# Kernel optimization log

Measured on AMD Instinct MI355X. Metric: run time of the kernel, lower is better.

Reference implementation:

```python
import jax, jax.numpy as jnp
import numpy as np

B, N, D, H = 4, 2048, 512, 8
HD = D // H
NUM_BUCKETS, MAX_EXACT, MAX_DIST = 44, 28, 2048
_BAND_RANGES = [range(38, 44), range(34, 40), range(28, 35), range(20, 28),
                range(13, 21), range(7, 14), range(3, 9), range(0, 6)]


def _band_mask():
    m = np.zeros((NUM_BUCKETS, H), dtype=np.float32)
    for h, band in enumerate(_BAND_RANGES):
        for j in band:
            m[j, h] = 1.0
    return jnp.asarray(m)


def _rel_bucket(n):
    # T5-style causal relative-position buckets: exact for d<MAX_EXACT, log-spaced above.
    i = jnp.arange(n)[:, None]
    j = jnp.arange(n)[None, :]
    d = jnp.maximum(i - j, 0)
    safe = jnp.maximum(d, 1).astype(jnp.float32)
    logb = MAX_EXACT + (jnp.log(safe / MAX_EXACT)
                        / np.log(MAX_DIST / MAX_EXACT)
                        * (NUM_BUCKETS - MAX_EXACT)).astype(jnp.int32)
    return jnp.where(d < MAX_EXACT, d, jnp.minimum(logb, NUM_BUCKETS - 1))  # [n,n]


def setup_inputs() -> dict:
    key = jax.random.key(0)
    ks = jax.random.split(key, 12)
    s = 0.02
    return {
        "x": jax.random.normal(ks[0], (B, N, D), jnp.float32),
        "k_delta": jax.random.normal(ks[1], (B, H, N, HD), jnp.float32) * 0.1,
        "v_delta": jax.random.normal(ks[2], (B, H, N, HD), jnp.float32) * 0.1,
        "qkv_w": jax.random.normal(ks[3], (D, 3 * D), jnp.float32) * s,
        "qkv_b": jnp.zeros((3 * D,), jnp.float32),
        "gate_w": jax.random.normal(ks[4], (D, D), jnp.float32) * s,
        "gate_b": jnp.zeros((D,), jnp.float32),
        "out_w": jax.random.normal(ks[5], (D, D), jnp.float32) * s,
        "out_b": jnp.zeros((D,), jnp.float32),
        "pos_bias": jax.random.normal(ks[6], (NUM_BUCKETS, H), jnp.float32) * 0.1,
        "if_gain": jnp.ones((H,), jnp.float32),
    }


def reference(x, k_delta, v_delta, qkv_w, qkv_b, gate_w, gate_b,
              out_w, out_b, pos_bias, if_gain):
    b, n, d = x.shape
    band = _band_mask()
    # hard per-head banding of the relative bias
    eff_bias = pos_bias * band + (1.0 - band) * (-100.0)           # [44,H]
    qkv = x @ qkv_w + qkv_b                                         # [B,N,3D]
    q, k, v = jnp.split(qkv, 3, axis=-1)
    q = q.reshape(b, n, H, HD).transpose(0, 2, 1, 3)                # [B,H,N,HD]
    k = k.reshape(b, n, H, HD).transpose(0, 2, 1, 3) + k_delta
    v = v.reshape(b, n, H, HD).transpose(0, 2, 1, 3) + v_delta
    bucket = _rel_bucket(n)                                         # [N,N] int
    bias = eff_bias[bucket].transpose(2, 0, 1)                      # [H,N,N]
    scores = jnp.einsum("bhid,bhjd->bhij", q, k) / np.sqrt(HD) + bias[None]
    causal = jnp.tril(jnp.ones((n, n), bool))
    scores = jnp.where(causal[None, None], scores, -1e9)
    attn = jax.nn.softmax(scores, axis=-1)
    out = jnp.einsum("bhij,bhjd->bhid", attn, v)                    # [B,H,N,HD]
    out = out * if_gain[None, :, None, None]                        # IF gain
    out_flat = out.transpose(0, 2, 1, 3).reshape(b, n, d)
    gate = jax.nn.sigmoid(x @ gate_w + gate_b)                      # output gating
    return (out_flat * gate) @ out_w + out_b
```

## Files before the change

kernel.cpp:

```cpp
#include <hip/hip_runtime.h>
#include <cmath>

typedef unsigned short u16;
typedef unsigned short u16x4 __attribute__((ext_vector_type(4)));
typedef unsigned short u16x8 __attribute__((ext_vector_type(8)));
typedef __bf16 bf16x8 __attribute__((ext_vector_type(8)));
typedef float f32x4 __attribute__((ext_vector_type(4)));

#define HNUM 8
#define HDIM 64
#define BATCH 4
#define NSEQ 2048
#define DMODEL 512
#define LP 72
#define CPE 264
#define NSLOT 14

__device__ __forceinline__ u16 f2bf(float f) {
  unsigned int u = __builtin_bit_cast(unsigned int, f);
  u += 0x7fffu + ((u >> 16) & 1u);
  return (u16)(u >> 16);
}

__device__ __forceinline__ float bf2f(u16 v) {
  unsigned int u = ((unsigned int)v) << 16;
  return __builtin_bit_cast(float, u);
}

__device__ __forceinline__ f32x4 mfma_bf16(u16x8 a, u16x8 b, f32x4 c) {
  return __builtin_amdgcn_mfma_f32_16x16x32_bf16(
      __builtin_bit_cast(bf16x8, a), __builtin_bit_cast(bf16x8, b), c, 0, 0, 0);
}

__device__ __forceinline__ void gload16(u16* lds, const u16* g) {
  __builtin_amdgcn_global_load_lds(
      (const __attribute__((address_space(1))) void*)g,
      (__attribute__((address_space(3))) void*)lds, 16, 0, 0);
}

__device__ __forceinline__ int swz_off(int row, int lg) {
  return row * 32 + ((lg ^ ((row >> 1) & 3)) << 3);
}

template <int ROWS>
__device__ __forceinline__ void stage_tile(u16* lds, const u16* g, int tid) {
  #pragma unroll
  for (int i = 0; i < ROWS / 64; ++i) {
    const int t = i * 256 + tid;
    const int row = t >> 2;
    const int ch = (t & 3) ^ ((row >> 1) & 3);
    gload16(lds + t * 8, g + (size_t)row * DMODEL + ch * 8);
  }
}

__device__ __forceinline__ void stageAB(u16* ldsA, u16* ldsB, const u16* gA,
                                        const u16* gB, int tid) {
  {
    const int s = tid;
    const int row = s >> 2;
    const int ch = (s & 3) ^ ((row >> 1) & 3);
    gload16(ldsA + s * 8, gA + (size_t)row * DMODEL + ch * 8);
  }
  #pragma unroll
  for (int i = 0; i < 2; ++i) {
    const int s = i * 512 + tid;
    const int row = s >> 2;
    const int ch = (s & 3) ^ ((row >> 1) & 3);
    gload16(ldsB + s * 8, gB + (size_t)row * DMODEL + ch * 8);
  }
}

__global__ __launch_bounds__(256) void cvt_bf16_kernel(
    const float* __restrict__ in, u16* __restrict__ out, int n8) {
  int i = blockIdx.x * 256 + threadIdx.x;
  if (i >= n8) return;
  const float4 f0 = *(const float4*)(in + i * 8);
  const float4 f1 = *(const float4*)(in + i * 8 + 4);
  u16x8 pk;
  pk[0] = f2bf(f0.x); pk[1] = f2bf(f0.y); pk[2] = f2bf(f0.z); pk[3] = f2bf(f0.w);
  pk[4] = f2bf(f1.x); pk[5] = f2bf(f1.y); pk[6] = f2bf(f1.z); pk[7] = f2bf(f1.w);
  *(u16x8*)(out + i * 8) = pk;
}

__global__ __launch_bounds__(256) void transpose_wall(
    const float* __restrict__ qkv_w, const float* __restrict__ gate_w,
    const float* __restrict__ out_w, u16* __restrict__ fused_wt,
    u16* __restrict__ out_wt) {
  __shared__ float tile[32][33];
  const int bx = blockIdx.x;
  const float* W;
  u16* Wt;
  int N, nb;
  if (bx < 48)      { W = qkv_w;  Wt = fused_wt;                     N = 1536; nb = bx; }
  else if (bx < 64) { W = gate_w; Wt = fused_wt + (size_t)1536 * 512; N = 512;  nb = bx - 48; }
  else              { W = out_w;  Wt = out_wt;                       N = 512;  nb = bx - 64; }
  const int n0 = nb * 32, k0 = blockIdx.y * 32;
  const int tx = threadIdx.x & 31, ty = threadIdx.x >> 5;
  #pragma unroll
  for (int yy = ty; yy < 32; yy += 8)
    tile[yy][tx] = W[(size_t)(k0 + yy) * N + n0 + tx];
  __syncthreads();
  #pragma unroll
  for (int yy = ty; yy < 32; yy += 8)
    Wt[(size_t)(n0 + yy) * DMODEL + k0 + tx] = f2bf(tile[tx][yy]);
}

__global__ __launch_bounds__(256) void transpose_v_kernel(
    const u16* __restrict__ v, u16* __restrict__ vT) {
  __shared__ u16 t[64][LP];
  const int n0 = blockIdx.x * 64;
  const size_t bh = blockIdx.y;
  const int r = threadIdx.x >> 2, c0 = (threadIdx.x & 3) << 4;
  const u16* src = v + (bh * NSEQ + n0 + r) * HDIM + c0;
  u16x8 a0 = *(const u16x8*)src;
  u16x8 a1 = *(const u16x8*)(src + 8);
  #pragma unroll
  for (int j = 0; j < 8; ++j) {
    t[c0 + j][r] = a0[j];
    t[c0 + 8 + j][r] = a1[j];
  }
  __syncthreads();
  u16x8 o0 = *(const u16x8*)&t[r][c0];
  u16x8 o1 = *(const u16x8*)&t[r][c0 + 8];
  u16* dst = vT + (bh * HDIM + r) * NSEQ + n0 + c0;
  *(u16x8*)dst = o0;
  *(u16x8*)(dst + 8) = o1;
}

__global__ __launch_bounds__(256) void bias_tab_kernel(
    const float* __restrict__ pos_bias, float* __restrict__ tab) {
  int d = blockIdx.x * 256 + threadIdx.x;
  if (d >= NSEQ) return;
  int bkt;
  if (d < 28) {
    bkt = d;
  } else {
    double t = log((double)d / 28.0) / log(2048.0 / 28.0) * 16.0;
    int ti = 28 + (int)t;
    bkt = ti < 43 ? ti : 43;
  }
  const int lo[8] = {38, 34, 28, 20, 13, 7, 3, 0};
  const int hi[8] = {44, 40, 35, 28, 21, 14, 9, 6};
  #pragma unroll
  for (int h = 0; h < HNUM; ++h) {
    bool inb = (bkt >= lo[h]) && (bkt < hi[h]);
    tab[h * NSEQ + d] = inb ? pos_bias[bkt * HNUM + h] : -100.0f;
  }
}

__global__ __launch_bounds__(512, 4) void gemm_fused(
    const u16* __restrict__ Abf, const u16* __restrict__ Wt,
    const float* __restrict__ qkv_b, const float* __restrict__ gate_b,
    const float* __restrict__ kdelta, const float* __restrict__ vdelta,
    u16* __restrict__ qbf, u16* __restrict__ kbf, u16* __restrict__ vbf,
    u16* __restrict__ gate) {
  __shared__ __align__(16) u16 S[36864];
  u16* SA3[3] = {S, S + 4096, S + 8192};
  u16* SB3[3] = {S + 12288, S + 20480, S + 28672};

  const int bid = blockIdx.x;
  const int xcd = bid & 7, loc = bid >> 3;
  const int m0 = (xcd * 8 + (loc & 7)) * 128;
  const int n0 = (loc >> 3) * 256;

  const int tid = threadIdx.x;
  const int w = tid >> 6, l = tid & 63, li = l & 15, lg = l >> 4;
  const int wm = w >> 2, wn = w & 3;

  f32x4 acc[4][4];
  #pragma unroll
  for (int i = 0; i < 4; ++i)
    #pragma unroll
    for (int j = 0; j < 4; ++j) acc[i][j] = f32x4{0.f, 0.f, 0.f, 0.f};

  const u16* Ab = Abf + (size_t)m0 * DMODEL;
  const u16* Bb = Wt + (size_t)n0 * DMODEL;

  stageAB(SA3[0], SB3[0], Ab, Bb, tid);
  stageAB(SA3[1], SB3[1], Ab + 32, Bb + 32, tid);

  #pragma unroll
  for (int kt = 0; kt < 16; ++kt) {
    if (kt <= 14) asm volatile("s_waitcnt vmcnt(3)" ::: "memory");
    else          asm volatile("s_waitcnt vmcnt(0)" ::: "memory");
    __builtin_amdgcn_s_barrier();
    __builtin_amdgcn_sched_barrier(0);
    if (kt + 2 < 16)
      stageAB(SA3[(kt + 2) % 3], SB3[(kt + 2) % 3],
              Ab + (kt + 2) * 32, Bb + (kt + 2) * 32, tid);
    const u16* Asb = SA3[kt % 3];
    const u16* Bsb = SB3[kt % 3];
    u16x8 af[4], bfr[4];
    #pragma unroll
    for (int mt = 0; mt < 4; ++mt)
      af[mt] = *(const u16x8*)&Asb[swz_off(wm * 64 + mt * 16 + li, lg)];
    #pragma unroll
    for (int nt = 0; nt < 4; ++nt)
      bfr[nt] = *(const u16x8*)&Bsb[swz_off(wn * 64 + nt * 16 + li, lg)];
    asm volatile("s_waitcnt lgkmcnt(0)" ::: "memory");
    __builtin_amdgcn_sched_barrier(0);
    #pragma unroll
    for (int mt = 0; mt < 4; ++mt)
      #pragma unroll
      for (int nt = 0; nt < 4; ++nt)
        acc[mt][nt] = mfma_bf16(af[mt], bfr[nt], acc[mt][nt]);
  }
  __syncthreads();

  u16* Ct = S;
  const int seg = n0 >> 9;
  const int nin = n0 & 511;
  #pragma unroll
  for (int nt = 0; nt < 4; ++nt) {
    const int col = wn * 64 + nt * 16 + li;
    const int colg = n0 + col;
    const float bv = (seg < 3) ? qkv_b[colg] : gate_b[colg & 511];
    #pragma unroll
    for (int mt = 0; mt < 4; ++mt) {
      const int row = wm * 64 + mt * 16 + lg * 4;
      #pragma unroll
      for (int r = 0; r < 4; ++r)
        Ct[(row + r) * CPE + col] = f2bf(acc[mt][nt][r] + bv);
    }
  }
  __syncthreads();

  #pragma unroll
  for (int p = 0; p < 8; ++p) {
    const int idx = p * 512 + tid;
    const int row = idx >> 5, ccol = (idx & 31) * 8;
    const int rg = m0 + row;
    const int bb = rg >> 11, n = rg & 2047;
    u16x8 cv = *(const u16x8*)&Ct[row * CPE + ccol];
    const int cws = nin + ccol;
    if (seg == 3) {
      u16x8 o;
      #pragma unroll
      for (int j = 0; j < 8; ++j)
        o[j] = f2bf(1.f / (1.f + __expf(-bf2f(cv[j]))));
      *(u16x8*)&gate[(size_t)rg * DMODEL + cws] = o;
    } else {
      const int hh = cws >> 6, hd = cws & 63;
      const size_t hidx = (((size_t)bb * HNUM + hh) * NSEQ + n) * HDIM + hd;
      if (seg == 0) {
        u16x8 o;
        #pragma unroll
        for (int j = 0; j < 8; ++j) o[j] = f2bf(bf2f(cv[j]) * 0.125f);
        *(u16x8*)&qbf[hidx] = o;
      } else {
        const float* dp = (seg == 1 ? kdelta : vdelta) + hidx;
        float4 d0 = *(const float4*)dp;
        float4 d1 = *(const float4*)(dp + 4);
        u16x8 o;
        o[0] = f2bf(bf2f(cv[0]) + d0.x); o[1] = f2bf(bf2f(cv[1]) + d0.y);
        o[2] = f2bf(bf2f(cv[2]) + d0.z); o[3] = f2bf(bf2f(cv[3]) + d0.w);
        o[4] = f2bf(bf2f(cv[4]) + d1.x); o[5] = f2bf(bf2f(cv[5]) + d1.y);
        o[6] = f2bf(bf2f(cv[6]) + d1.z); o[7] = f2bf(bf2f(cv[7]) + d1.w);
        *(u16x8*)&((seg == 1) ? kbf : vbf)[hidx] = o;
      }
    }
  }
}

__global__ __launch_bounds__(256) void gemm_out(
    const u16* __restrict__ Abf, const u16* __restrict__ Wt,
    const float* __restrict__ bias, float* __restrict__ outf) {
  __shared__ __align__(16) u16 As[3][64 * 32];
  __shared__ __align__(16) u16 Bs[3][128 * 32];

  const int m0 = blockIdx.y * 64, n0 = blockIdx.x * 128;
  const int tid = threadIdx.x;
  const int w = tid >> 6, l = tid & 63, li = l & 15, lg = l >> 4;
  const int wr = w >> 1, wc = w & 1;

  f32x4 acc[2][4];
  #pragma unroll
  for (int i = 0; i < 2; ++i)
    #pragma unroll
    for (int j = 0; j < 4; ++j) acc[i][j] = f32x4{0.f, 0.f, 0.f, 0.f};

  const u16* Ab = Abf + (size_t)m0 * DMODEL;
  const u16* Bb = Wt + (size_t)n0 * DMODEL;

  stage_tile<64>(As[0], Ab, tid);
  stage_tile<128>(Bs[0], Bb, tid);
  stage_tile<64>(As[1], Ab + 32, tid);
  stage_tile<128>(Bs[1], Bb + 32, tid);

  #pragma unroll
  for (int kt = 0; kt < 16; ++kt) {
    if (kt <= 14) asm volatile("s_waitcnt vmcnt(3)" ::: "memory");
    else          asm volatile("s_waitcnt vmcnt(0)" ::: "memory");
    __builtin_amdgcn_s_barrier();
    __builtin_amdgcn_sched_barrier(0);
    if (kt + 2 < 16) {
      stage_tile<64>(As[(kt + 2) % 3], Ab + (kt + 2) * 32, tid);
      stage_tile<128>(Bs[(kt + 2) % 3], Bb + (kt + 2) * 32, tid);
    }
    const u16* Asb = As[kt % 3];
    const u16* Bsb = Bs[kt % 3];
    u16x8 af[2], bfr[4];
    #pragma unroll
    for (int mt = 0; mt < 2; ++mt)
      af[mt] = *(const u16x8*)&Asb[swz_off(wr * 32 + mt * 16 + li, lg)];
    #pragma unroll
    for (int nt = 0; nt < 4; ++nt)
      bfr[nt] = *(const u16x8*)&Bsb[swz_off(wc * 64 + nt * 16 + li, lg)];
    asm volatile("s_waitcnt lgkmcnt(0)" ::: "memory");
    __builtin_amdgcn_sched_barrier(0);
    #pragma unroll
    for (int mt = 0; mt < 2; ++mt)
      #pragma unroll
      for (int nt = 0; nt < 4; ++nt)
        acc[mt][nt] = mfma_bf16(af[mt], bfr[nt], acc[mt][nt]);
  }

  #pragma unroll
  for (int nt = 0; nt < 4; ++nt) {
    const int colg = n0 + wc * 64 + nt * 16 + li;
    const float bv = bias[colg];
    #pragma unroll
    for (int mt = 0; mt < 2; ++mt) {
      #pragma unroll
      for (int r = 0; r < 4; ++r) {
        const int rowg = m0 + wr * 32 + mt * 16 + lg * 4 + r;
        outf[(size_t)rowg * DMODEL + colg] = acc[mt][nt][r] + bv;
      }
    }
  }
}

__global__ __launch_bounds__(256) void attn_kernel(
    const u16* __restrict__ qbf, const u16* __restrict__ kbf,
    const u16* __restrict__ vbfT, const float* __restrict__ bias_tab,
    const float* __restrict__ if_gain, const u16* __restrict__ gate,
    u16* __restrict__ attn_out, u16* __restrict__ partO,
    float* __restrict__ partM, float* __restrict__ partL) {
  __shared__ __align__(16) u16 Ks[64][LP];
  __shared__ __align__(16) u16 Vt[64][LP];
  __shared__ __align__(16) u16 Pl[4][16][LP];

  static const int DMINW[8] = {408, 139, 26, 18, 11, 5, 1, 0};
  static const int DMAXW[8] = {2049, 702, 185, 29, 22, 15, 10, 7};
  static const int DMINS[8] = {412, 143, 30, 22, 15, 9, 5, 2};
  static const int SH[19] = {0,0,0,0,0,0,0,0, 1,1,1,1, 2,2, 3,4,5,6,7};
  static const int SC[19] = {0,1,2,3,4,5,6,7, 0,1,2,3, 0,1, 0,0,0,0,0};
  static const int SN[19] = {8,8,8,8,8,8,8,8, 4,4,4,4, 2,2, 1,1,1,1,1};

  const int slot = blockIdx.x >> 7;
  const int rem = blockIdx.x & 127;
  const int qt = 31 - (rem >> 2);
  const int b = rem & 3;
  const int h = SH[slot], ch = SC[slot], nc = SN[slot];
  const int bh = b * HNUM + h;
  const int q0 = qt * 64;
  const int tid = threadIdx.x;
  const int w = tid >> 6, l = tid & 63, li = l & 15, lg = l >> 4;

  const u16* qrow = qbf + ((size_t)bh * NSEQ + q0 + w * 16 + li) * HDIM;
  u16x8 qf0 = *(const u16x8*)(qrow + lg * 8);
  u16x8 qf1 = *(const u16x8*)(qrow + 32 + lg * 8);

  const bool pure = q0 >= DMINS[h];
  int kv_lo = 0, kv_hi = q0 + 64;
  if (pure) {
    int lo = q0 - DMAXW[h];
    kv_lo = (lo > 0 ? lo : 0) & ~63;
    kv_hi = q0 + 64 - DMINW[h];
  }
  const int t0 = kv_lo >> 6, t1 = (kv_hi - 1) >> 6;
  const int len = t1 - t0 + 1;
  const int ta = t0 + (len * ch) / nc;
  const int tb = t0 + (len * (ch + 1)) / nc - 1;

  const int srow = tid >> 2;
  const int scb = (tid & 3) << 4;
  const float* btab = bias_tab + h * NSEQ;

  float mrun = -INFINITY, lrun = 0.f;
  f32x4 O[4] = {{0.f,0.f,0.f,0.f},{0.f,0.f,0.f,0.f},
                {0.f,0.f,0.f,0.f},{0.f,0.f,0.f,0.f}};

  for (int tt = ta; tt <= tb; ++tt) {
    const int kv0 = tt << 6;
    {
      const size_t kbase = ((size_t)bh * NSEQ + kv0 + srow) * HDIM + scb;
      u16x8 k0 = *(const u16x8*)(kbf + kbase);
      u16x8 k1 = *(const u16x8*)(kbf + kbase + 8);
      const size_t vbase = ((size_t)bh * HDIM + srow) * NSEQ + kv0 + scb;
      u16x8 v0 = *(const u16x8*)(vbfT + vbase);
      u16x8 v1 = *(const u16x8*)(vbfT + vbase + 8);
      *(u16x8*)&Ks[srow][scb] = k0;
      *(u16x8*)&Ks[srow][scb + 8] = k1;
      *(u16x8*)&Vt[srow][scb] = v0;
      *(u16x8*)&Vt[srow][scb + 8] = v1;
    }
    __syncthreads();

    f32x4 s[4];
    #pragma unroll
    for (int t = 0; t < 4; ++t) {
      u16x8 a0 = *(const u16x8*)&Ks[t * 16 + li][lg * 8];
      u16x8 a1 = *(const u16x8*)&Ks[t * 16 + li][32 + lg * 8];
      f32x4 acc = {0.f, 0.f, 0.f, 0.f};
      acc = mfma_bf16(a0, qf0, acc);
      acc = mfma_bf16(a1, qf1, acc);
      s[t] = acc;
    }

    const int D0 = (q0 + w * 16 + li) - kv0 - lg * 4;
    float rm = -1e30f;
    #pragma unroll
    for (int t = 0; t < 4; ++t) {
      #pragma unroll
      for (int r = 0; r < 4; ++r) {
        int d = D0 - 16 * t - r;
        float sv = s[t][r];
        sv = (d >= 0) ? (sv + btab[d]) : -1e30f;
        s[t][r] = sv;
        rm = fmaxf(rm, sv);
      }
    }
    rm = fmaxf(rm, __shfl_xor(rm, 16, 64));
    rm = fmaxf(rm, __shfl_xor(rm, 32, 64));
    const float mn = fmaxf(mrun, rm);
    const float f = __expf(mrun - mn);
    mrun = mn;
    float ps = 0.f;
    #pragma unroll
    for (int t = 0; t < 4; ++t) {
      #pragma unroll
      for (int r = 0; r < 4; ++r) {
        float p = __expf(s[t][r] - mn);
        s[t][r] = p;
        ps += p;
      }
    }
    ps += __shfl_xor(ps, 16, 64);
    ps += __shfl_xor(ps, 32, 64);
    lrun = lrun * f + ps;

    #pragma unroll
    for (int t = 0; t < 4; ++t) {
      u16x4 pk;
      pk[0] = f2bf(s[t][0]); pk[1] = f2bf(s[t][1]);
      pk[2] = f2bf(s[t][2]); pk[3] = f2bf(s[t][3]);
      *(u16x4*)&Pl[w][li][t * 16 + lg * 4] = pk;
    }

    float fr[4];
    #pragma unroll
    for (int r = 0; r < 4; ++r) fr[r] = __shfl(f, lg * 4 + r, 64);
    #pragma unroll
    for (int dt = 0; dt < 4; ++dt) {
      O[dt][0] *= fr[0]; O[dt][1] *= fr[1];
      O[dt][2] *= fr[2]; O[dt][3] *= fr[3];
    }
    __syncthreads();

    #pragma unroll
    for (int ks = 0; ks < 2; ++ks) {
      u16x8 pA = *(const u16x8*)&Pl[w][li][ks * 32 + lg * 8];
      #pragma unroll
      for (int dt = 0; dt < 4; ++dt) {
        u16x8 vB = *(const u16x8*)&Vt[dt * 16 + li][ks * 32 + lg * 8];
        O[dt] = mfma_bf16(pA, vB, O[dt]);
      }
    }
    __syncthreads();
  }

  if (nc == 1) {
    const float gain = if_gain[h];
    float linv[4];
    #pragma unroll
    for (int r = 0; r < 4; ++r)
      linv[r] = gain / __shfl(lrun, lg * 4 + r, 64);
    #pragma unroll
    for (int r = 0; r < 4; ++r) {
      const int i = q0 + w * 16 + lg * 4 + r;
      const size_t base = ((size_t)b * NSEQ + i) * DMODEL + h * HDIM + li;
      #pragma unroll
      for (int dt = 0; dt < 4; ++dt) {
        const float g = bf2f(gate[base + dt * 16]);
        attn_out[base + dt * 16] = f2bf(O[dt][r] * linv[r] * g);
      }
    }
  } else {
    const int sbase = (b * 32 + qt) * NSLOT + slot;
    #pragma unroll
    for (int r = 0; r < 4; ++r) {
      const int rl = w * 16 + lg * 4 + r;
      #pragma unroll
      for (int dt = 0; dt < 4; ++dt)
        partO[(size_t)sbase * 4096 + rl * 64 + dt * 16 + li] = f2bf(O[dt][r]);
    }
    if (lg == 0) {
      partM[sbase * 64 + w * 16 + li] = mrun;
      partL[sbase * 64 + w * 16 + li] = lrun;
    }
  }
}

__global__ __launch_bounds__(256) void combine_kernel(
    const u16* __restrict__ partO, const float* __restrict__ partM,
    const float* __restrict__ partL, const float* __restrict__ if_gain,
    const u16* __restrict__ gate, u16* __restrict__ attn_out) {
  const int b = blockIdx.x & 3, qt = blockIdx.x >> 2;
  const int tid = threadIdx.x;
  const int row = tid >> 2, d0 = (tid & 3) << 4;
  static const int HNC[3] = {8, 4, 2};
  static const int HS0[3] = {0, 8, 12};

  #pragma unroll
  for (int hc = 0; hc < 3; ++hc) {
    const int nc = HNC[hc], s0 = HS0[hc];
    const int sbase = (b * 32 + qt) * NSLOT + s0;
    float m[8];
    float M = -INFINITY;
    #pragma unroll
    for (int c = 0; c < 8; ++c) {
      m[c] = (c < nc) ? partM[(sbase + c) * 64 + row] : -INFINITY;
      M = fmaxf(M, m[c]);
    }
    float wch[8];
    float den = 0.f;
    #pragma unroll
    for (int c = 0; c < 8; ++c) {
      wch[c] = (c < nc) ? __expf(m[c] - M) : 0.f;
      if (c < nc) den += wch[c] * partL[(sbase + c) * 64 + row];
    }
    float num[16];
    #pragma unroll
    for (int j = 0; j < 16; ++j) num[j] = 0.f;
    #pragma unroll
    for (int c = 0; c < 8; ++c) {
      if (c < nc) {
        const u16* op = partO + (size_t)(sbase + c) * 4096 + row * 64 + d0;
        u16x8 o0 = *(const u16x8*)op;
        u16x8 o1 = *(const u16x8*)(op + 8);
        #pragma unroll
        for (int j = 0; j < 8; ++j) {
          num[j]     += wch[c] * bf2f(o0[j]);
          num[8 + j] += wch[c] * bf2f(o1[j]);
        }
      }
    }
    const float inv = if_gain[hc] / den;
    const size_t obase =
        ((size_t)b * NSEQ + qt * 64 + row) * DMODEL + hc * HDIM + d0;
    u16x8 g0 = *(const u16x8*)(gate + obase);
    u16x8 g1 = *(const u16x8*)(gate + obase + 8);
    u16x8 r0, r1;
    #pragma unroll
    for (int j = 0; j < 8; ++j) {
      r0[j] = f2bf(num[j] * inv * bf2f(g0[j]));
      r1[j] = f2bf(num[8 + j] * inv * bf2f(g1[j]));
    }
    *(u16x8*)(attn_out + obase) = r0;
    *(u16x8*)(attn_out + obase + 8) = r1;
  }
}

extern "C" void kernel_launch(void* const* d_in, const int* in_sizes, int n_in,
                              void* d_out, int out_size, void* d_ws,
                              size_t ws_size, hipStream_t stream) {
  const float* x       = (const float*)d_in[0];
  const float* k_delta = (const float*)d_in[1];
  const float* v_delta = (const float*)d_in[2];
  const float* qkv_w   = (const float*)d_in[3];
  const float* qkv_b   = (const float*)d_in[4];
  const float* gate_w  = (const float*)d_in[5];
  const float* gate_b  = (const float*)d_in[6];
  const float* out_w   = (const float*)d_in[7];
  const float* out_b   = (const float*)d_in[8];
  const float* pos_bias = (const float*)d_in[9];
  const float* if_gain  = (const float*)d_in[10];
  float* out = (float*)d_out;
  char* ws = (char*)d_ws;

  u16*   xbf      = (u16*)(ws + 0);
  u16*   qbf      = (u16*)(ws + 8388608);
  u16*   kbf      = (u16*)(ws + 16777216);
  u16*   vbf      = (u16*)(ws + 25165824);
  u16*   vbfT     = (u16*)(ws + 33554432);
  u16*   gate_buf = (u16*)(ws + 41943040);
  u16*   fused_wt = (u16*)(ws + 50331648);
  u16*   out_wt   = (u16*)(ws + 52428800);
  float* bias_tab = (float*)(ws + 52953088);
  u16*   partO = (u16*)(ws + 53018624);
  float* partM = (float*)(ws + 67698688);
  float* partL = (float*)(ws + 68157440);
  u16*   attn_buf = vbf;

  cvt_bf16_kernel<<<dim3(2048), dim3(256), 0, stream>>>(
      x, xbf, BATCH * NSEQ * DMODEL / 8);
  transpose_wall<<<dim3(80, 16), dim3(256), 0, stream>>>(
      qkv_w, gate_w, out_w, fused_wt, out_wt);
  bias_tab_kernel<<<dim3(8), dim3(256), 0, stream>>>(pos_bias, bias_tab);

  gemm_fused<<<dim3(512), dim3(512), 0, stream>>>(
      xbf, fused_wt, qkv_b, gate_b, k_delta, v_delta,
      qbf, kbf, vbf, gate_buf);

  transpose_v_kernel<<<dim3(32, 32), dim3(256), 0, stream>>>(vbf, vbfT);

  attn_kernel<<<dim3(2432), dim3(256), 0, stream>>>(
      qbf, kbf, vbfT, bias_tab, if_gain, gate_buf, attn_buf,
      partO, partM, partL);

  combine_kernel<<<dim3(128), dim3(256), 0, stream>>>(
      partO, partM, partL, if_gain, gate_buf, attn_buf);

  gemm_out<<<dim3(4, 128), dim3(256), 0, stream>>>(
      attn_buf, out_wt, out_b, out);

  (void)in_sizes; (void)n_in; (void)out_size; (void)ws_size;
}
```

Before: 92.61 us.

## Load K/V MFMA fragments directly from global memory, drop shared staging and block barriers

After: 119.6 us. 1.29x slower.

```diff
diff --git a/kernel.cpp b/kernel.cpp
--- a/kernel.cpp
+++ b/kernel.cpp
@@ -336,8 +336,6 @@
     const float* __restrict__ if_gain, const u16* __restrict__ gate,
     u16* __restrict__ attn_out, u16* __restrict__ partO,
     float* __restrict__ partM, float* __restrict__ partL) {
-  __shared__ __align__(16) u16 Ks[64][LP];
-  __shared__ __align__(16) u16 Vt[64][LP];
   __shared__ __align__(16) u16 Pl[4][16][LP];
 
   static const int DMINW[8] = {408, 139, 26, 18, 11, 5, 1, 0};
@@ -373,9 +371,9 @@
   const int ta = t0 + (len * ch) / nc;
   const int tb = t0 + (len * (ch + 1)) / nc - 1;
 
-  const int srow = tid >> 2;
-  const int scb = (tid & 3) << 4;
   const float* btab = bias_tab + h * NSEQ;
+  const u16* kfrag = kbf + ((size_t)bh * NSEQ + li) * HDIM + lg * 8;
+  const u16* vfrag = vbfT + ((size_t)bh * HDIM + li) * NSEQ + lg * 8;
 
   float mrun = -INFINITY, lrun = 0.f;
   f32x4 O[4] = {{0.f,0.f,0.f,0.f},{0.f,0.f,0.f,0.f},
@@ -383,25 +381,13 @@
 
   for (int tt = ta; tt <= tb; ++tt) {
     const int kv0 = tt << 6;
-    {
-      const size_t kbase = ((size_t)bh * NSEQ + kv0 + srow) * HDIM + scb;
-      u16x8 k0 = *(const u16x8*)(kbf + kbase);
-      u16x8 k1 = *(const u16x8*)(kbf + kbase + 8);
-      const size_t vbase = ((size_t)bh * HDIM + srow) * NSEQ + kv0 + scb;
-      u16x8 v0 = *(const u16x8*)(vbfT + vbase);
-      u16x8 v1 = *(const u16x8*)(vbfT + vbase + 8);
-      *(u16x8*)&Ks[srow][scb] = k0;
-      *(u16x8*)&Ks[srow][scb + 8] = k1;
-      *(u16x8*)&Vt[srow][scb] = v0;
-      *(u16x8*)&Vt[srow][scb + 8] = v1;
-    }
-    __syncthreads();
 
     f32x4 s[4];
     #pragma unroll
     for (int t = 0; t < 4; ++t) {
-      u16x8 a0 = *(const u16x8*)&Ks[t * 16 + li][lg * 8];
-      u16x8 a1 = *(const u16x8*)&Ks[t * 16 + li][32 + lg * 8];
+      const u16* kp = kfrag + (size_t)(kv0 + t * 16) * HDIM;
+      u16x8 a0 = *(const u16x8*)kp;
+      u16x8 a1 = *(const u16x8*)(kp + 32);
       f32x4 acc = {0.f, 0.f, 0.f, 0.f};
       acc = mfma_bf16(a0, qf0, acc);
       acc = mfma_bf16(a1, qf1, acc);
@@ -456,18 +442,22 @@
       O[dt][0] *= fr[0]; O[dt][1] *= fr[1];
       O[dt][2] *= fr[2]; O[dt][3] *= fr[3];
     }
-    __syncthreads();
+
+    asm volatile("s_waitcnt lgkmcnt(0)" ::: "memory");
+    __builtin_amdgcn_sched_barrier(0);
 
     #pragma unroll
     for (int ks = 0; ks < 2; ++ks) {
       u16x8 pA = *(const u16x8*)&Pl[w][li][ks * 32 + lg * 8];
       #pragma unroll
       for (int dt = 0; dt < 4; ++dt) {
-        u16x8 vB = *(const u16x8*)&Vt[dt * 16 + li][ks * 32 + lg * 8];
+        u16x8 vB = *(const u16x8*)(vfrag + (size_t)(dt * 16) * NSEQ +
+                                   kv0 + ks * 32);
         O[dt] = mfma_bf16(pA, vB, O[dt]);
       }
     }
-    __syncthreads();
+    asm volatile("s_waitcnt lgkmcnt(0)" ::: "memory");
+    __builtin_amdgcn_sched_barrier(0);
   }
 
   if (nc == 1) {
```
